# Optimization experiments

Measured on AMD Instinct MI355X. Metric: run time of the kernel, lower is better.

## Reference

```python
import jax, jax.numpy as jnp
import numpy as np
import math

T = 32
DIM = 1024
BATCH = 4096
ETA = 1.0


def setup_inputs() -> dict:
    key = jax.random.key(0)
    k1, k2, k3, k4 = jax.random.split(key, 4)
    x = jax.random.normal(k1, (BATCH, DIM), dtype=jnp.float32)
    mu = jax.random.uniform(k2, (T, DIM), dtype=jnp.float32, minval=-0.5, maxval=0.5)
    rho = jax.random.uniform(k3, (T, DIM), dtype=jnp.float32, minval=-0.5, maxval=0.5)
    # stochastic Beta(gamma_1, gamma_2) draws in the original (scipy beta.rvs);
    # passed as an explicit input, kept strictly inside (0, 1)
    beta_samples = jax.random.uniform(k4, (BATCH, T), dtype=jnp.float32,
                                      minval=0.01, maxval=0.99)
    return {"x": x, "mu": mu, "rho": rho, "beta_samples": beta_samples}


def _forward(x, mu, rho, beta_samples):
    B, D = x.shape
    Tn = mu.shape[0]
    log2pi = math.log(2.0 * math.pi)

    std = jnp.log1p(jnp.exp(rho))              # [T, D]
    log_std_sum = jnp.sum(jnp.log(std), axis=-1)   # [T]
    inv_var = 1.0 / (std * std)                # [T, D]

    # Diagonal Gaussian log-prob, batched over all T components via GEMMs
    quad = (jnp.einsum('bd,td->bt', x * x, inv_var)
            - 2.0 * jnp.einsum('bd,td->bt', x, mu * inv_var)
            + jnp.sum(mu * mu * inv_var, axis=-1)[None, :])   # [B, T]
    log_pdfs = -0.5 * D * log2pi - log_std_sum[None, :] - 0.5 * quad  # [B, T]

    # entropy of each diagonal Gaussian, broadcast to batch
    entropy = (D / 2.0) * (log2pi + 1.0) + log_std_sum   # [T]
    entropy = jnp.broadcast_to(entropy[None, :], (B, Tn))

    # stick-breaking weights: pi = mix_weights(beta)[:, :-1]
    beta1m_cumprod = jnp.cumprod(1.0 - beta_samples, axis=-1)   # [B, T]
    pi = beta_samples * jnp.concatenate(
        [jnp.ones((B, 1), x.dtype), beta1m_cumprod[:, :-1]], axis=-1)  # [B, T]
    log_pi = jnp.log(pi)

    # get_phi
    kl_gaussian = log_pdfs + entropy            # [B, T]
    N_t_gaussian = jnp.sum(kl_gaussian, axis=0, keepdims=True)  # [1, T]
    N_t_pi = jnp.sum(log_pi, axis=0, keepdims=True)             # [1, T]
    mix = N_t_pi / (N_t_gaussian + N_t_pi)      # [1, T]
    kl = mix * kl_gaussian + (1.0 - mix) * log_pi
    phi_new = jax.nn.softmax(kl, axis=1)        # [B, T]
    kl_g_mixed = mix * kl_gaussian              # [B, T]

    likelihood = jnp.mean(jnp.sum(phi_new * kl_g_mixed, axis=1), axis=0)  # scalar
    return likelihood


def reference(x, mu, rho, beta_samples):
    return _forward(x, mu, rho, beta_samples)
```

## Files before the change

### kernel.cpp

```cpp
#include <hip/hip_runtime.h>
#include <math.h>

constexpr int NT = 32;
constexpr int ND = 1024;
constexpr int NB = 4096;
constexpr int NBLK_MAIN = 512;

constexpr int OFF_M2C = 32768;
constexpr int OFF_C2  = 65536;
constexpr int OFF_KLG = 65664;
constexpr int OFF_LPI = 196736;
constexpr int OFF_PG  = 327808;
constexpr int OFF_PP  = 344192;

__global__ __launch_bounds__(256) void k_stats(const float* __restrict__ mu,
                                               const float* __restrict__ rho,
                                               float* __restrict__ ws,
                                               float* __restrict__ out) {
  float* ivc = ws;
  float* m2c = ws + OFF_M2C;
  float* c2  = ws + OFF_C2;

  const int t = blockIdx.x;
  const int c = threadIdx.x;

  float4 mu4  = reinterpret_cast<const float4*>(mu  + t * ND)[c];
  float4 rho4 = reinterpret_cast<const float4*>(rho + t * ND)[c];

  float rr[4] = {rho4.x, rho4.y, rho4.z, rho4.w};
  float mm[4] = {mu4.x,  mu4.y,  mu4.z,  mu4.w};
  float iv[4], m2[4];
  float c2p = 0.0f;
#pragma unroll
  for (int j = 0; j < 4; ++j) {
    float sd  = log1pf(expf(rr[j]));
    float ivv = 1.0f / (sd * sd);
    iv[j] = ivv;
    m2[j] = -2.0f * mm[j] * ivv;
    c2p  += mm[j] * mm[j] * ivv;
  }
  float4 iv4 = {iv[0], iv[1], iv[2], iv[3]};
  float4 m24 = {m2[0], m2[1], m2[2], m2[3]};
  reinterpret_cast<float4*>(ivc)[c * NT + t] = iv4;
  reinterpret_cast<float4*>(m2c)[c * NT + t] = m24;

#pragma unroll
  for (int m = 32; m >= 1; m >>= 1) c2p += __shfl_xor(c2p, m, 64);
  __shared__ float red[4];
  const int wave = threadIdx.x >> 6, lane = threadIdx.x & 63;
  if (lane == 0) red[wave] = c2p;
  __syncthreads();
  if (threadIdx.x == 0) {
    c2[t] = red[0] + red[1] + red[2] + red[3];
    if (t == 0) out[0] = 0.0f;
  }
}

__global__ __launch_bounds__(512, 4) void k_main(const float* __restrict__ x,
                                                 const float* __restrict__ beta,
                                                 float* __restrict__ ws) {
  const float* ivc = ws;
  const float* m2c = ws + OFF_M2C;
  const float* c2  = ws + OFF_C2;
  float* klg = ws + OFF_KLG;
  float* lpi = ws + OFF_LPI;
  float* Pg  = ws + OFF_PG;
  float* Pp  = ws + OFF_PP;

  const int tid  = threadIdx.x;
  const int q    = tid >> 6;
  const int lane = tid & 63;
  const int h = lane >> 5, t = lane & 31;
  const int row0 = blockIdx.x * 8;

  __shared__ float xs[8 * 1024];
  __shared__ float part[8][8][32];

  {
    const float4* xg4 = reinterpret_cast<const float4*>(x) + (size_t)row0 * 256;
    float4* xs4w = reinterpret_cast<float4*>(xs);
#pragma unroll
    for (int k = 0; k < 4; ++k) {
      xs4w[k * 512 + tid] = xg4[k * 512 + tid];
    }
  }
  __syncthreads();

  const int c0 = q * 32 + h * 16;
  const float4* ivp = reinterpret_cast<const float4*>(ivc) + (size_t)c0 * NT + t;
  const float4* m2p = reinterpret_cast<const float4*>(m2c) + (size_t)c0 * NT + t;
  const float4* xs4 = reinterpret_cast<const float4*>(xs) + c0;

  float a[8] = {0.f, 0.f, 0.f, 0.f, 0.f, 0.f, 0.f, 0.f};
#pragma unroll 4
  for (int i = 0; i < 16; ++i) {
    float4 iv4 = ivp[(size_t)i * NT];
    float4 m24 = m2p[(size_t)i * NT];
#pragma unroll
    for (int r = 0; r < 8; ++r) {
      float4 xv = xs4[r * 256 + i];
      a[r] = fmaf(xv.x, fmaf(xv.x, iv4.x, m24.x), a[r]);
      a[r] = fmaf(xv.y, fmaf(xv.y, iv4.y, m24.y), a[r]);
      a[r] = fmaf(xv.z, fmaf(xv.z, iv4.z, m24.z), a[r]);
      a[r] = fmaf(xv.w, fmaf(xv.w, iv4.w, m24.w), a[r]);
    }
  }
#pragma unroll
  for (int r = 0; r < 8; ++r) a[r] += __shfl_xor(a[r], 32, 64);

  if (h == 0) {
#pragma unroll
    for (int r = 0; r < 8; ++r) part[q][r][t] = a[r];
  }
  __syncthreads();

  const int rr = tid >> 5, t2 = tid & 31;
  float kv = 0.f, lp = 0.f;
  if (tid < 256) {
    float quad = 0.f;
#pragma unroll
    for (int qq = 0; qq < 8; ++qq) quad += part[qq][rr][t2];
    kv = 512.0f - 0.5f * (quad + c2[t2]);
    klg[(size_t)(row0 + rr) * NT + t2] = kv;

    const float b = beta[(size_t)(row0 + rr) * NT + t2];
    const float l1m = log1pf(-b);
    float s = l1m;
#pragma unroll
    for (int d = 1; d < 32; d <<= 1) {
      float v = __shfl_up(s, (unsigned)d, 32);
      if (t2 >= d) s += v;
    }
    lp = logf(b) + (s - l1m);
    lpi[(size_t)(row0 + rr) * NT + t2] = lp;
  }
  __syncthreads();
  if (tid < 256) {
    part[0][rr][t2] = kv;
    part[1][rr][t2] = lp;
  }
  __syncthreads();
  if (tid < 32) {
    float sg = 0.f, sp = 0.f;
#pragma unroll
    for (int r = 0; r < 8; ++r) { sg += part[0][r][tid]; sp += part[1][r][tid]; }
    Pg[(size_t)blockIdx.x * NT + tid] = sg;
    Pp[(size_t)blockIdx.x * NT + tid] = sp;
  }
}

__global__ __launch_bounds__(512) void k_final(const float* __restrict__ ws,
                                               float* __restrict__ out) {
  const float* klg = ws + OFF_KLG;
  const float* lpi = ws + OFF_LPI;
  const float* Pg  = ws + OFF_PG;
  const float* Pp  = ws + OFF_PP;

  const int tid  = threadIdx.x;
  const int wave = tid >> 6, lane = tid & 63;
  const int t = tid & 31;
  const int g = tid >> 5;

  __shared__ float ngF[32], npF[32];
  __shared__ float redG[8][32], redP[8][32];
  __shared__ float red[8];

  {
    float sg = 0.f, sp = 0.f;
#pragma unroll 8
    for (int b = g; b < NBLK_MAIN; b += 16) {
      sg += Pg[(size_t)b * NT + t];
      sp += Pp[(size_t)b * NT + t];
    }
    sg += __shfl_xor(sg, 32, 64);
    sp += __shfl_xor(sp, 32, 64);
    if (lane < 32) { redG[wave][t] = sg; redP[wave][t] = sp; }
  }
  __syncthreads();
  if (tid < 32) {
    float ng = 0.f, np = 0.f;
#pragma unroll
    for (int w = 0; w < 8; ++w) { ng += redG[w][tid]; np += redP[w][tid]; }
    ngF[tid] = ng;
    npF[tid] = np;
  }
  __syncthreads();

  const int row = blockIdx.x * 16 + g;
  const float kg = klg[(size_t)row * NT + t];
  const float lp = lpi[(size_t)row * NT + t];
  const float ng = ngF[t], np = npF[t];
  const float mix  = np / (ng + np);
  const float klgm = mix * kg;
  const float kl   = klgm + (1.0f - mix) * lp;

  float m = kl;
#pragma unroll
  for (int mk = 16; mk >= 1; mk >>= 1) m = fmaxf(m, __shfl_xor(m, mk, 64));
  const float e = expf(kl - m);
  float num = e * klgm, den = e;
#pragma unroll
  for (int mk = 16; mk >= 1; mk >>= 1) {
    num += __shfl_xor(num, mk, 64);
    den += __shfl_xor(den, mk, 64);
  }
  float s = num / den;
  s += __shfl_xor(s, 32, 64);

  if (lane == 0) red[wave] = s;
  __syncthreads();
  if (tid == 0) {
    float tot = 0.f;
#pragma unroll
    for (int w = 0; w < 8; ++w) tot += red[w];
    atomicAdd(out, tot * (1.0f / (float)NB));
  }
}

extern "C" void kernel_launch(void* const* d_in, const int* in_sizes, int n_in,
                              void* d_out, int out_size, void* d_ws, size_t ws_size,
                              hipStream_t stream) {
  const float* x    = (const float*)d_in[0];
  const float* mu   = (const float*)d_in[1];
  const float* rho  = (const float*)d_in[2];
  const float* beta = (const float*)d_in[3];
  float* out = (float*)d_out;
  float* ws  = (float*)d_ws;

  hipLaunchKernelGGL(k_stats, dim3(32),        dim3(256), 0, stream, mu, rho, ws, out);
  hipLaunchKernelGGL(k_main,  dim3(NBLK_MAIN), dim3(512), 0, stream, x, beta, ws);
  hipLaunchKernelGGL(k_final, dim3(256),       dim3(512), 0, stream, ws, out);
}
```

Baseline: 29.02 us.

## Split quadratic-form reduction into D-slices with LDS-staged stats and separate reduce kernel

The main kernel is restructured so each block handles 64 rows over one 128-wide slice of D. The inv_var and mu-term stats for that slice are staged in shared memory instead of being read from global memory by every block. Per-slice partial quads go to a new workspace buffer, and a new k_mid kernel sums the slices, computes klg and log_pi, and writes the block partials. This improves reuse of the stats tiles, at the cost of an extra kernel launch and a 4 MB partial-sum round trip through memory.

Result: slower. 31.09 us (+7.2%).

```diff
diff --git a/kernel.cpp b/kernel.cpp
--- a/kernel.cpp
+++ b/kernel.cpp
@@ -4,14 +4,17 @@
 constexpr int NT = 32;
 constexpr int ND = 1024;
 constexpr int NB = 4096;
-constexpr int NBLK_MAIN = 512;
+constexpr int NSLICE = 8;
+constexpr int NRG   = 64;
+constexpr int NBLK_MID = 256;
 
 constexpr int OFF_M2C = 32768;
 constexpr int OFF_C2  = 65536;
-constexpr int OFF_KLG = 65664;
-constexpr int OFF_LPI = 196736;
-constexpr int OFF_PG  = 327808;
-constexpr int OFF_PP  = 344192;
+constexpr int OFF_KLG = 65600;
+constexpr int OFF_LPI = 196672;
+constexpr int OFF_QP  = 327744;
+constexpr int OFF_PG  = 1376320;
+constexpr int OFF_PP  = 1384512;
 
 __global__ __launch_bounds__(256) void k_stats(const float* __restrict__ mu,
                                                const float* __restrict__ rho,
@@ -56,94 +59,117 @@
   }
 }
 
-__global__ __launch_bounds__(512, 4) void k_main(const float* __restrict__ x,
-                                                 const float* __restrict__ beta,
-                                                 float* __restrict__ ws) {
-  const float* ivc = ws;
-  const float* m2c = ws + OFF_M2C;
-  const float* c2  = ws + OFF_C2;
+__global__ __launch_bounds__(512, 4) void k_slice(const float* __restrict__ x,
+                                                  float* __restrict__ ws) {
+  float* qp = ws + OFF_QP;
+
+  const int bid   = blockIdx.x;
+  const int slice = bid >> 6;
+  const int rg    = bid & 63;
+  const int tid   = threadIdx.x;
+
+  __shared__ float xs[64 * 128];
+  __shared__ float ivs[32 * 32 * 4];
+  __shared__ float m2s[32 * 32 * 4];
+
+  {
+    const float4* xg4 = reinterpret_cast<const float4*>(x);
+    float4* xs4w = reinterpret_cast<float4*>(xs);
+    const int row = tid >> 3;
+    const int j0  = tid & 7;
+#pragma unroll
+    for (int p = 0; p < 4; ++p) {
+      const int j = j0 + 8 * p;
+      xs4w[row * 32 + j] =
+          xg4[(size_t)(rg * 64 + row) * 256 + slice * 32 + j];
+    }
+  }
+  {
+    const float4* ivg = reinterpret_cast<const float4*>(ws) + (size_t)slice * 1024;
+    const float4* m2g = reinterpret_cast<const float4*>(ws + OFF_M2C) + (size_t)slice * 1024;
+    float4* ivw = reinterpret_cast<float4*>(ivs);
+    float4* m2w = reinterpret_cast<float4*>(m2s);
+    ivw[tid]       = ivg[tid];
+    ivw[tid + 512] = ivg[tid + 512];
+    m2w[tid]       = m2g[tid];
+    m2w[tid + 512] = m2g[tid + 512];
+  }
+  __syncthreads();
+
+  const int q    = tid >> 6;
+  const int lane = tid & 63;
+  const int h = lane >> 5, t = lane & 31;
+  const float4* ivs4 = reinterpret_cast<const float4*>(ivs);
+  const float4* m2s4 = reinterpret_cast<const float4*>(m2s);
+  const float4* xsr  = reinterpret_cast<const float4*>(xs) + (size_t)(q * 8) * 32;
+
+  float a[8] = {0.f, 0.f, 0.f, 0.f, 0.f, 0.f, 0.f, 0.f};
+#pragma unroll 2
+  for (int i = 0; i < 16; ++i) {
+    const int c = h * 16 + i;
+    float4 iv4 = ivs4[c * 32 + t];
+    float4 m24 = m2s4[c * 32 + t];
+#pragma unroll
+    for (int r = 0; r < 8; ++r) {
+      float4 xv = xsr[r * 32 + c];
+      a[r] = fmaf(xv.x, fmaf(xv.x, iv4.x, m24.x), a[r]);
+      a[r] = fmaf(xv.y, fmaf(xv.y, iv4.y, m24.y), a[r]);
+      a[r] = fmaf(xv.z, fmaf(xv.z, iv4.z, m24.z), a[r]);
+      a[r] = fmaf(xv.w, fmaf(xv.w, iv4.w, m24.w), a[r]);
+    }
+  }
+#pragma unroll
+  for (int r = 0; r < 8; ++r) a[r] += __shfl_xor(a[r], 32, 64);
+
+  if (h == 0) {
+#pragma unroll
+    for (int r = 0; r < 8; ++r) {
+      const int row = rg * 64 + q * 8 + r;
+      qp[((size_t)slice * NB + row) * NT + t] = a[r];
+    }
+  }
+}
+
+__global__ __launch_bounds__(512) void k_mid(const float* __restrict__ beta,
+                                             float* __restrict__ ws) {
+  const float* c2 = ws + OFF_C2;
+  const float* qp = ws + OFF_QP;
   float* klg = ws + OFF_KLG;
   float* lpi = ws + OFF_LPI;
   float* Pg  = ws + OFF_PG;
   float* Pp  = ws + OFF_PP;
 
-  const int tid  = threadIdx.x;
-  const int q    = tid >> 6;
-  const int lane = tid & 63;
-  const int h = lane >> 5, t = lane & 31;
-  const int row0 = blockIdx.x * 8;
-
-  __shared__ float xs[8 * 1024];
-  __shared__ float part[8][8][32];
-
-  {
-    const float4* xg4 = reinterpret_cast<const float4*>(x) + (size_t)row0 * 256;
-    float4* xs4w = reinterpret_cast<float4*>(xs);
-#pragma unroll
-    for (int k = 0; k < 4; ++k) {
-      xs4w[k * 512 + tid] = xg4[k * 512 + tid];
-    }
-  }
-  __syncthreads();
-
-  const int c0 = q * 32 + h * 16;
-  const float4* ivp = reinterpret_cast<const float4*>(ivc) + (size_t)c0 * NT + t;
-  const float4* m2p = reinterpret_cast<const float4*>(m2c) + (size_t)c0 * NT + t;
-  const float4* xs4 = reinterpret_cast<const float4*>(xs) + c0;
-
-  float a[8] = {0.f, 0.f, 0.f, 0.f, 0.f, 0.f, 0.f, 0.f};
-#pragma unroll 4
-  for (int i = 0; i < 16; ++i) {
-    float4 iv4 = ivp[(size_t)i * NT];
-    float4 m24 = m2p[(size_t)i * NT];
-#pragma unroll
-    for (int r = 0; r < 8; ++r) {
-      float4 xv = xs4[r * 256 + i];
-      a[r] = fmaf(xv.x, fmaf(xv.x, iv4.x, m24.x), a[r]);
-      a[r] = fmaf(xv.y, fmaf(xv.y, iv4.y, m24.y), a[r]);
-      a[r] = fmaf(xv.z, fmaf(xv.z, iv4.z, m24.z), a[r]);
-      a[r] = fmaf(xv.w, fmaf(xv.w, iv4.w, m24.w), a[r]);
-    }
-  }
-#pragma unroll
-  for (int r = 0; r < 8; ++r) a[r] += __shfl_xor(a[r], 32, 64);
-
-  if (h == 0) {
-#pragma unroll
-    for (int r = 0; r < 8; ++r) part[q][r][t] = a[r];
-  }
-  __syncthreads();
-
-  const int rr = tid >> 5, t2 = tid & 31;
-  float kv = 0.f, lp = 0.f;
-  if (tid < 256) {
-    float quad = 0.f;
-#pragma unroll
-    for (int qq = 0; qq < 8; ++qq) quad += part[qq][rr][t2];
-    kv = 512.0f - 0.5f * (quad + c2[t2]);
-    klg[(size_t)(row0 + rr) * NT + t2] = kv;
-
-    const float b = beta[(size_t)(row0 + rr) * NT + t2];
-    const float l1m = log1pf(-b);
-    float s = l1m;
-#pragma unroll
-    for (int d = 1; d < 32; d <<= 1) {
-      float v = __shfl_up(s, (unsigned)d, 32);
-      if (t2 >= d) s += v;
-    }
-    lp = logf(b) + (s - l1m);
-    lpi[(size_t)(row0 + rr) * NT + t2] = lp;
-  }
-  __syncthreads();
-  if (tid < 256) {
-    part[0][rr][t2] = kv;
-    part[1][rr][t2] = lp;
-  }
+  const int tid = threadIdx.x;
+  const int rr = tid >> 5, t = tid & 31;
+  const int row = blockIdx.x * 16 + rr;
+
+  float quad = 0.f;
+#pragma unroll
+  for (int s = 0; s < NSLICE; ++s)
+    quad += qp[((size_t)s * NB + row) * NT + t];
+
+  const float kv = 512.0f - 0.5f * (quad + c2[t]);
+  klg[(size_t)row * NT + t] = kv;
+
+  const float b = beta[(size_t)row * NT + t];
+  const float l1m = log1pf(-b);
+  float s = l1m;
+#pragma unroll
+  for (int d = 1; d < 32; d <<= 1) {
+    float v = __shfl_up(s, (unsigned)d, 32);
+    if (t >= d) s += v;
+  }
+  const float lp = logf(b) + (s - l1m);
+  lpi[(size_t)row * NT + t] = lp;
+
+  __shared__ float klP[16][32], lpP[16][32];
+  klP[rr][t] = kv;
+  lpP[rr][t] = lp;
   __syncthreads();
   if (tid < 32) {
     float sg = 0.f, sp = 0.f;
 #pragma unroll
-    for (int r = 0; r < 8; ++r) { sg += part[0][r][tid]; sp += part[1][r][tid]; }
+    for (int r = 0; r < 16; ++r) { sg += klP[r][tid]; sp += lpP[r][tid]; }
     Pg[(size_t)blockIdx.x * NT + tid] = sg;
     Pp[(size_t)blockIdx.x * NT + tid] = sp;
   }
@@ -167,8 +193,8 @@
 
   {
     float sg = 0.f, sp = 0.f;
-#pragma unroll 8
-    for (int b = g; b < NBLK_MAIN; b += 16) {
+#pragma unroll 4
+    for (int b = g; b < NBLK_MID; b += 16) {
       sg += Pg[(size_t)b * NT + t];
       sp += Pp[(size_t)b * NT + t];
     }
@@ -227,7 +253,8 @@
   float* out = (float*)d_out;
   float* ws  = (float*)d_ws;
 
-  hipLaunchKernelGGL(k_stats, dim3(32),        dim3(256), 0, stream, mu, rho, ws, out);
-  hipLaunchKernelGGL(k_main,  dim3(NBLK_MAIN), dim3(512), 0, stream, x, beta, ws);
-  hipLaunchKernelGGL(k_final, dim3(256),       dim3(512), 0, stream, ws, out);
-}
+  hipLaunchKernelGGL(k_stats, dim3(32),  dim3(256), 0, stream, mu, rho, ws, out);
+  hipLaunchKernelGGL(k_slice, dim3(NSLICE * NRG), dim3(512), 0, stream, x, ws);
+  hipLaunchKernelGGL(k_mid,   dim3(NBLK_MID), dim3(512), 0, stream, beta, ws);
+  hipLaunchKernelGGL(k_final, dim3(256), dim3(512), 0, stream, ws, out);
+}
```

## Process 16 rows per block with 1024 threads and packed f2 FMAs

Applied to the files above, without the earlier changes.

The main kernel now handles 16 batch rows per block with 1024 threads (256 blocks instead of 512). Each lane covers 8 float4 columns, so every loaded inverse-variance and mean coefficient is reused across twice as many rows. The inner accumulation uses two-wide vector FMAs so the compiler can emit packed FP32 instructions. The cost is 64KB of LDS per block and more accumulator registers, which lowers occupancy, and the main loop is left unrolled only once.

After: 29.63 us. 1.02x slower.

```diff
diff --git a/kernel.cpp b/kernel.cpp
--- a/kernel.cpp
+++ b/kernel.cpp
@@ -4,14 +4,17 @@
 constexpr int NT = 32;
 constexpr int ND = 1024;
 constexpr int NB = 4096;
-constexpr int NBLK_MAIN = 512;
+constexpr int ROWS = 16;
+constexpr int NBLK_MAIN = NB / ROWS;
+
+typedef float f2 __attribute__((ext_vector_type(2)));
 
 constexpr int OFF_M2C = 32768;
 constexpr int OFF_C2  = 65536;
-constexpr int OFF_KLG = 65664;
-constexpr int OFF_LPI = 196736;
-constexpr int OFF_PG  = 327808;
-constexpr int OFF_PP  = 344192;
+constexpr int OFF_KLG = 65600;
+constexpr int OFF_LPI = 196672;
+constexpr int OFF_PG  = 327744;
+constexpr int OFF_PP  = 335936;
 
 __global__ __launch_bounds__(256) void k_stats(const float* __restrict__ mu,
                                                const float* __restrict__ rho,
@@ -56,9 +59,9 @@
   }
 }
 
-__global__ __launch_bounds__(512, 4) void k_main(const float* __restrict__ x,
-                                                 const float* __restrict__ beta,
-                                                 float* __restrict__ ws) {
+__global__ __launch_bounds__(1024, 4) void k_main(const float* __restrict__ x,
+                                                  const float* __restrict__ beta,
+                                                  float* __restrict__ ws) {
   const float* ivc = ws;
   const float* m2c = ws + OFF_M2C;
   const float* c2  = ws + OFF_C2;
@@ -71,55 +74,58 @@
   const int q    = tid >> 6;
   const int lane = tid & 63;
   const int h = lane >> 5, t = lane & 31;
-  const int row0 = blockIdx.x * 8;
-
-  __shared__ float xs[8 * 1024];
-  __shared__ float part[8][8][32];
+  const int row0 = blockIdx.x * ROWS;
+
+  __shared__ float xs[ROWS * ND];
+  __shared__ float part[16][ROWS][32];
 
   {
     const float4* xg4 = reinterpret_cast<const float4*>(x) + (size_t)row0 * 256;
     float4* xs4w = reinterpret_cast<float4*>(xs);
 #pragma unroll
     for (int k = 0; k < 4; ++k) {
-      xs4w[k * 512 + tid] = xg4[k * 512 + tid];
-    }
-  }
-  __syncthreads();
-
-  const int c0 = q * 32 + h * 16;
+      xs4w[k * 1024 + tid] = xg4[k * 1024 + tid];
+    }
+  }
+  __syncthreads();
+
+  const int c0 = q * 16 + h * 8;
   const float4* ivp = reinterpret_cast<const float4*>(ivc) + (size_t)c0 * NT + t;
   const float4* m2p = reinterpret_cast<const float4*>(m2c) + (size_t)c0 * NT + t;
   const float4* xs4 = reinterpret_cast<const float4*>(xs) + c0;
 
-  float a[8] = {0.f, 0.f, 0.f, 0.f, 0.f, 0.f, 0.f, 0.f};
-#pragma unroll 4
-  for (int i = 0; i < 16; ++i) {
+  f2 a2[ROWS];
+#pragma unroll
+  for (int r = 0; r < ROWS; ++r) a2[r] = (f2){0.f, 0.f};
+
+#pragma unroll 1
+  for (int i = 0; i < 8; ++i) {
     float4 iv4 = ivp[(size_t)i * NT];
     float4 m24 = m2p[(size_t)i * NT];
-#pragma unroll
-    for (int r = 0; r < 8; ++r) {
+    const f2 ivl = {iv4.x, iv4.y}, ivh = {iv4.z, iv4.w};
+    const f2 ml  = {m24.x, m24.y}, mh  = {m24.z, m24.w};
+#pragma unroll
+    for (int r = 0; r < ROWS; ++r) {
       float4 xv = xs4[r * 256 + i];
-      a[r] = fmaf(xv.x, fmaf(xv.x, iv4.x, m24.x), a[r]);
-      a[r] = fmaf(xv.y, fmaf(xv.y, iv4.y, m24.y), a[r]);
-      a[r] = fmaf(xv.z, fmaf(xv.z, iv4.z, m24.z), a[r]);
-      a[r] = fmaf(xv.w, fmaf(xv.w, iv4.w, m24.w), a[r]);
-    }
-  }
-#pragma unroll
-  for (int r = 0; r < 8; ++r) a[r] += __shfl_xor(a[r], 32, 64);
-
-  if (h == 0) {
-#pragma unroll
-    for (int r = 0; r < 8; ++r) part[q][r][t] = a[r];
+      const f2 xl = {xv.x, xv.y}, xh = {xv.z, xv.w};
+      a2[r] = __builtin_elementwise_fma(xl, __builtin_elementwise_fma(xl, ivl, ml), a2[r]);
+      a2[r] = __builtin_elementwise_fma(xh, __builtin_elementwise_fma(xh, ivh, mh), a2[r]);
+    }
+  }
+#pragma unroll
+  for (int r = 0; r < ROWS; ++r) {
+    float s = a2[r].x + a2[r].y;
+    s += __shfl_xor(s, 32, 64);
+    if (h == 0) part[q][r][t] = s;
   }
   __syncthreads();
 
   const int rr = tid >> 5, t2 = tid & 31;
   float kv = 0.f, lp = 0.f;
-  if (tid < 256) {
+  if (tid < 512) {
     float quad = 0.f;
 #pragma unroll
-    for (int qq = 0; qq < 8; ++qq) quad += part[qq][rr][t2];
+    for (int w = 0; w < 16; ++w) quad += part[w][rr][t2];
     kv = 512.0f - 0.5f * (quad + c2[t2]);
     klg[(size_t)(row0 + rr) * NT + t2] = kv;
 
@@ -135,7 +141,7 @@
     lpi[(size_t)(row0 + rr) * NT + t2] = lp;
   }
   __syncthreads();
-  if (tid < 256) {
+  if (tid < 512) {
     part[0][rr][t2] = kv;
     part[1][rr][t2] = lp;
   }
@@ -143,7 +149,7 @@
   if (tid < 32) {
     float sg = 0.f, sp = 0.f;
 #pragma unroll
-    for (int r = 0; r < 8; ++r) { sg += part[0][r][tid]; sp += part[1][r][tid]; }
+    for (int r = 0; r < ROWS; ++r) { sg += part[0][r][tid]; sp += part[1][r][tid]; }
     Pg[(size_t)blockIdx.x * NT + tid] = sg;
     Pp[(size_t)blockIdx.x * NT + tid] = sp;
   }
@@ -167,7 +173,7 @@
 
   {
     float sg = 0.f, sp = 0.f;
-#pragma unroll 8
+#pragma unroll 4
     for (int b = g; b < NBLK_MAIN; b += 16) {
       sg += Pg[(size_t)b * NT + t];
       sp += Pp[(size_t)b * NT + t];
@@ -227,7 +233,7 @@
   float* out = (float*)d_out;
   float* ws  = (float*)d_ws;
 
-  hipLaunchKernelGGL(k_stats, dim3(32),        dim3(256), 0, stream, mu, rho, ws, out);
-  hipLaunchKernelGGL(k_main,  dim3(NBLK_MAIN), dim3(512), 0, stream, x, beta, ws);
-  hipLaunchKernelGGL(k_final, dim3(256),       dim3(512), 0, stream, ws, out);
-}
+  hipLaunchKernelGGL(k_stats, dim3(32),        dim3(256),  0, stream, mu, rho, ws, out);
+  hipLaunchKernelGGL(k_main,  dim3(NBLK_MAIN), dim3(1024), 0, stream, x, beta, ws);
+  hipLaunchKernelGGL(k_final, dim3(256),       dim3(512),  0, stream, ws, out);
+}
```
